# Kernel optimization log

Measured on AMD Instinct MI355X. Metric: run time of the kernel, lower is better.

Reference implementation:

```python
import jax, jax.numpy as jnp
import numpy as np

FS = 50000000.0
PI = jnp.pi


def _scale_matrix(alpha, kW, n_pad):
    """kW x kW matrix equal to torch linear-interp (align_corners=False)
    kW -> N -> kW with N = round(kW / clamp(alpha, 0.001)), N bounded by n_pad."""
    a = jnp.maximum(alpha, 0.001)
    N = jnp.clip(jnp.round(kW / a), 1, n_pad).astype(jnp.int32)
    Nf = N.astype(jnp.float32)
    eye_k = jnp.eye(kW, dtype=jnp.float32)
    eye_n = jnp.eye(n_pad, dtype=jnp.float32)
    # down-sample matrix D: length kW -> N (rows j >= N masked to 0)
    j = jnp.arange(n_pad, dtype=jnp.float32)
    c = jnp.maximum((j + 0.5) * (kW / Nf) - 0.5, 0.0)
    i0f = jnp.floor(c)
    w1 = c - i0f
    i0 = jnp.clip(i0f.astype(jnp.int32), 0, kW - 1)
    i1 = jnp.minimum(i0 + 1, kW - 1)
    D = (1.0 - w1)[:, None] * eye_k[i0] + w1[:, None] * eye_k[i1]
    D = D * (jnp.arange(n_pad) < N)[:, None]
    # up-sample matrix U: length N -> kW (reads only cols < N)
    i = jnp.arange(kW, dtype=jnp.float32)
    c2 = jnp.maximum((i + 0.5) * (Nf / kW) - 0.5, 0.0)
    j0 = jnp.floor(c2).astype(jnp.int32)
    j1 = jnp.minimum(j0 + 1, N - 1)
    w2 = c2 - j0.astype(jnp.float32)
    U = (1.0 - w2)[:, None] * eye_n[j0] + w2[:, None] * eye_n[j1]
    return U @ D  # [kW, kW]


def _mix_phase(w, phi):
    # w: [B,OC,2,1,kW], phi: [B,kW]; complex rotation of (I,Q) channel pair
    I, Q = w[:, :, 0, 0, :], w[:, :, 1, 0, :]
    c, sn = jnp.cos(phi)[:, None, :], jnp.sin(phi)[:, None, :]
    return jnp.stack([I * c - Q * sn, I * sn + Q * c], axis=2)[:, :, :, None, :]


def _steered_kernels(z, s, base_w, B):
    OC, IC, _, kW = base_w.shape
    n_pad = 2 * kW
    sf = jnp.nan_to_num(s)
    act = z > 0
    pick = lambda idx, neutral: jnp.where(act[:, idx], sf[:, idx], neutral)
    wB = jnp.broadcast_to(base_w[None], (B, OC, IC, 1, kW))
    # SCALE (PERTURB_ORDER idx 1)
    alpha = pick(1, 1.0)
    M = jax.vmap(lambda a: _scale_matrix(a, kW, n_pad))(alpha)  # [B,kW,kW]
    wB = jnp.einsum('bij,bocuj->bocui', M, wB)
    # CFO (idx 0) then CHIRP (idx 4): sequential phase rotations = summed phase
    n = jnp.arange(kW, dtype=jnp.float32)
    phi = 2.0 * PI * pick(0, 0.0)[:, None] * n[None, :] / FS
    t = n / FS
    phi = phi + PI * pick(4, 0.0)[:, None] * (t ** 2)[None, :]
    wB = _mix_phase(wB, phi)
    # GAIN (idx 2)
    wB = pick(2, 1.0)[:, None, None, None, None] * wB
    # SHIFT (idx 3): per-sample circular roll, out[i] = in[(i - s) mod kW]
    sh = jnp.round(pick(3, 0.0)).astype(jnp.int32)
    idx = (jnp.arange(kW)[None, :] - sh[:, None]) % kW  # [B,kW]
    idx = jnp.broadcast_to(idx[:, None, None, None, :], wB.shape)
    wB = jnp.take_along_axis(wB, idx, axis=-1)
    return wB  # [B,OC,2,1,kW]


def reference(x, z, s, base_w):
    B, IC, _, L = x.shape
    OC, _, _, kW = base_w.shape
    wB = _steered_kernels(z, s, base_w, B)
    xG = x.reshape(1, B * IC, 1, L)
    wG = wB.reshape(B * OC, IC, 1, kW)
    y = jax.lax.conv_general_dilated(
        xG, wG, window_strides=(1, 1), padding=[(0, 0), (kW // 2, kW // 2)],
        dimension_numbers=('NCHW', 'OIHW', 'NCHW'), feature_group_count=B)
    return y.reshape(B, OC, 1, L)


def setup_inputs() -> dict:
    key = jax.random.key(0)
    ks = jax.random.split(key, 4)
    B, OC, IC, kW, L = 32, 64, 2, 65, 65536
    x = jax.random.normal(ks[0], (B, IC, 1, L), dtype=jnp.float32)
    base_w = jax.random.normal(ks[1], (OC, IC, 1, kW), dtype=jnp.float32) * 0.1
    z = jax.random.randint(ks[2], (B, 5), 0, 2).astype(jnp.int32)
    u = jax.random.uniform(ks[3], (B, 5), dtype=jnp.float32)
    f0 = (u[:, 0] * 2.0 - 1.0) * 1.0e5         # CFO in +/-100 kHz
    alpha = 0.75 + u[:, 1] * 0.65               # SCALE in [0.75, 1.4]
    gain = 0.5 + u[:, 2]                        # GAIN in [0.5, 1.5]
    shift = jnp.round((u[:, 3] * 2.0 - 1.0) * 3.0)  # SHIFT integer in [-3, 3]
    chirp = (u[:, 4] * 2.0 - 1.0) * 1.0e12      # CHIRP rate
    s = jnp.stack([f0, alpha, gain, shift, chirp], axis=1)
    return {"x": x, "z": z, "s": s, "base_w": base_w}
```

## Files before the change

kernel.cpp:

```cpp
#include <hip/hip_runtime.h>
#include <math.h>

#define KW 65
#define L_LEN 65536
#define B_N 32
#define OC_N 64
#define KPAD 160
#define SEC 80
#define LT 256
#define XBASE 344

typedef __attribute__((ext_vector_type(8))) short short8;
typedef __attribute__((ext_vector_type(4))) float f32x4;

__device__ __forceinline__ unsigned short f2bf(float f) {
    unsigned u = __builtin_bit_cast(unsigned, f);
    unsigned r = u + 0x7FFFu + ((u >> 16) & 1u);
    return (unsigned short)(r >> 16);
}

__device__ __forceinline__ float nan0(float v) {
    if (isnan(v)) return 0.0f;
    if (isinf(v)) return v > 0.0f ? 3.4028234663852886e38f : -3.4028234663852886e38f;
    return v;
}

__global__ __launch_bounds__(256) void steer_weights(
        const int* __restrict__ z, const float* __restrict__ s,
        const float* __restrict__ bw, unsigned short* __restrict__ wpk) {
    const float PI = 3.14159265358979323846f;
    const float FS = 50000000.0f;
    int b = blockIdx.x;
    int t = threadIdx.x;

    const int*   zb = z + b * 5;
    const float* sb = s + b * 5;
    float f0    = (zb[0] > 0) ? nan0(sb[0]) : 0.0f;
    float alpha = (zb[1] > 0) ? nan0(sb[1]) : 1.0f;
    float gain  = (zb[2] > 0) ? nan0(sb[2]) : 1.0f;
    float shf   = (zb[3] > 0) ? nan0(sb[3]) : 0.0f;
    float chirp = (zb[4] > 0) ? nan0(sb[4]) : 0.0f;

    float a = fmaxf(alpha, 0.001f);
    float Nf_raw = rintf(65.0f / a);
    int   N  = (int)fminf(fmaxf(Nf_raw, 1.0f), 130.0f);
    float Nf = (float)N;
    int   sh = (int)rintf(shf);

    __shared__ float rw[OC_N][2][KW];
    __shared__ float cph[KW], sph[KW];

    if (t < KW) {
        float n  = (float)t;
        float tt = n / FS;
        float phi = 2.0f * PI * f0 * n / FS + PI * chirp * tt * tt;
        cph[t] = cosf(phi);
        sph[t] = sinf(phi);
    }
    if (t >= 128) {
        int oc = (t - 128) >> 1, ch = t & 1;
        const float* w = bw + (oc * 2 + ch) * KW;
        float KdivN = 65.0f / Nf;
        float NdivK = Nf / 65.0f;
        for (int i = 0; i < KW; ++i) {
            float c2  = fmaxf(((float)i + 0.5f) * NdivK - 0.5f, 0.0f);
            float j0f = floorf(c2);
            int   j0  = (int)j0f;
            int   j1  = min(j0 + 1, N - 1);
            float w2  = c2 - j0f;
            float v0, v1;
            {
                float c   = fmaxf(((float)j0 + 0.5f) * KdivN - 0.5f, 0.0f);
                float i0f = floorf(c);
                int   i0  = min((int)i0f, KW - 1);
                int   i1  = min(i0 + 1, KW - 1);
                float w1  = c - i0f;
                v0 = (1.0f - w1) * w[i0] + w1 * w[i1];
            }
            {
                float c   = fmaxf(((float)j1 + 0.5f) * KdivN - 0.5f, 0.0f);
                float i0f = floorf(c);
                int   i0  = min((int)i0f, KW - 1);
                int   i1  = min(i0 + 1, KW - 1);
                float w1  = c - i0f;
                v1 = (1.0f - w1) * w[i0] + w1 * w[i1];
            }
            rw[oc][ch][i] = (1.0f - w2) * v0 + w2 * v1;
        }
    }
    __syncthreads();
    {
        int oc = t >> 2, q = t & 3;
        unsigned short* ob = wpk + ((size_t)b * OC_N + oc) * KPAD;
        int sh0 = ((sh % KW) + KW) % KW;
        int k0 = 17 * q, k1 = min(KW, k0 + 17);
        for (int k = k0; k < k1; ++k) {
            float I = rw[oc][0][k], Q = rw[oc][1][k];
            float cp = cph[k], sp = sph[k];
            float Ip = (I * cp - Q * sp) * gain;
            float Qp = (I * sp + Q * cp) * gain;
            int kk = k + sh0; if (kk >= KW) kk -= KW;
            ob[kk]       = f2bf(Ip);
            ob[SEC + kk] = f2bf(Qp);
        }
        if (q == 3) {
            for (int kk = KW; kk < SEC; ++kk) { ob[kk] = 0; ob[SEC + kk] = 0; }
        }
    }
}

__global__ __launch_bounds__(256, 3) void steer_conv_mfma(
        const float* __restrict__ x, const unsigned short* __restrict__ wpk,
        float* __restrict__ y) {
    int b   = blockIdx.y;
    int l0  = blockIdx.x * LT;
    int tid = threadIdx.x;
    int wv = tid >> 6, lane = tid & 63;
    int c = lane & 15, g = lane >> 4;
    int a = wv & 1, lsub = wv >> 1;

    __shared__ __align__(16) unsigned short xt[8][2][XBASE];

    short8 afr[2][5];
    #pragma unroll
    for (int ot = 0; ot < 2; ++ot) {
        const unsigned short* wb = wpk + ((size_t)b * OC_N + 32 * a + 16 * ot + c) * KPAD;
        #pragma unroll
        for (int s = 0; s < 5; ++s)
            afr[ot][s] = *(const short8*)(wb + 32 * s + 8 * g);
    }

    const float* xb = x + (size_t)b * 2 * L_LEN;

    if (tid < 172) {
        int ch = tid / 86, i4 = tid % 86;
        int gi = l0 - 32 + 4 * i4;
        float4 v;
        if (gi >= 0 && gi + 3 < L_LEN) {
            v = *(const float4*)(xb + (size_t)ch * L_LEN + gi);
        } else {
            float tmp[4];
            #pragma unroll
            for (int u = 0; u < 4; ++u) {
                int q = gi + u;
                tmp[u] = (q >= 0 && q < L_LEN) ? xb[(size_t)ch * L_LEN + q] : 0.0f;
            }
            v = make_float4(tmp[0], tmp[1], tmp[2], tmp[3]);
        }
        unsigned r0 = (unsigned)f2bf(v.x) | ((unsigned)f2bf(v.y) << 16);
        unsigned r1 = (unsigned)f2bf(v.z) | ((unsigned)f2bf(v.w) << 16);
        *(uint2*)&xt[0][ch][4 * i4] = make_uint2(r0, r1);
    }
    __syncthreads();

    if (tid < 84) {
        int ch = tid / 42, j = tid % 42;
        const unsigned* src = (const unsigned*)&xt[0][ch][8 * j];
        unsigned d[8];
        #pragma unroll
        for (int i = 0; i < 8; ++i) d[i] = src[i];
        #pragma unroll
        for (int p = 1; p < 8; ++p) {
            int q = p >> 1;
            unsigned o[4];
            #pragma unroll
            for (int i = 0; i < 4; ++i)
                o[i] = (p & 1) ? ((d[i + q] >> 16) | (d[i + q + 1] << 16)) : d[i + q];
            *(uint4*)&xt[p][ch][8 * j] = make_uint4(o[0], o[1], o[2], o[3]);
        }
    }

    int boff[5];
    #pragma unroll
    for (int s = 0; s < 5; ++s) {
        int k0 = 32 * s + 8 * g;
        int ch = (k0 >= SEC) ? 1 : 0;
        int t0 = k0 - SEC * ch;
        boff[s] = ch * XBASE + 128 * lsub + 8 * c + t0;
    }
    __syncthreads();

    f32x4 acc[2][8];
    #pragma unroll
    for (int ot = 0; ot < 2; ++ot)
        #pragma unroll
        for (int p = 0; p < 8; ++p) acc[ot][p] = (f32x4){0.f, 0.f, 0.f, 0.f};

    #pragma unroll
    for (int p = 0; p < 8; ++p) {
        const unsigned short* xp = &xt[p][0][0];
        #pragma unroll
        for (int s = 0; s < 5; ++s) {
            short8 bfr = *(const short8*)(xp + boff[s]);
            acc[0][p] = __builtin_amdgcn_mfma_f32_16x16x32_bf16(afr[0][s], bfr, acc[0][p], 0, 0, 0);
            acc[1][p] = __builtin_amdgcn_mfma_f32_16x16x32_bf16(afr[1][s], bfr, acc[1][p], 0, 0, 0);
        }
    }

    #pragma unroll
    for (int ot = 0; ot < 2; ++ot) {
        #pragma unroll
        for (int r = 0; r < 4; ++r) {
            int oc = 32 * a + 16 * ot + 4 * g + r;
            float* yr = y + ((size_t)b * OC_N + oc) * L_LEN + l0 + 128 * lsub + 8 * c;
            f32x4 lo = { acc[ot][0][r], acc[ot][1][r], acc[ot][2][r], acc[ot][3][r] };
            f32x4 hi = { acc[ot][4][r], acc[ot][5][r], acc[ot][6][r], acc[ot][7][r] };
            *(f32x4*)yr       = lo;
            *((f32x4*)yr + 1) = hi;
        }
    }
}

extern "C" void kernel_launch(void* const* d_in, const int* in_sizes, int n_in,
                              void* d_out, int out_size, void* d_ws, size_t ws_size,
                              hipStream_t stream) {
    const float* x  = (const float*)d_in[0];
    const int*   z  = (const int*)d_in[1];
    const float* s  = (const float*)d_in[2];
    const float* bw = (const float*)d_in[3];
    float* y = (float*)d_out;
    unsigned short* wpk = (unsigned short*)d_ws;

    steer_weights<<<dim3(B_N), dim3(256), 0, stream>>>(z, s, bw, wpk);
    steer_conv_mfma<<<dim3(L_LEN / LT, B_N), dim3(256), 0, stream>>>(x, wpk, y);
}
```

Before: 147.3 us.

## Loop conv blocks over four tiles with prefetch and parallelize weight resampling

Each conv block now processes four consecutive 256-sample tiles in a loop. The input LDS buffer is double-buffered, and the global load for the next tile is issued by the non-shift threads while the shift/pack step of the current tile runs, so per-block setup (weight fragment loads) is amortized and input fetch latency overlaps other work. The weight kernel precomputes interpolation index and weight tables in shared memory, then spreads the 128x65 resampling over all 256 threads instead of a 65-step serial loop on 128 threads. The cost is a quarter as many conv blocks and more LDS per block.

After: 142.2 us. 3.5% less time.

```diff
diff --git a/kernel.cpp b/kernel.cpp
--- a/kernel.cpp
+++ b/kernel.cpp
@@ -8,6 +8,8 @@
 #define KPAD 160
 #define SEC 80
 #define LT 256
+#define NT 4
+#define LGRP (LT*NT)
 #define XBASE 344
 
 typedef __attribute__((ext_vector_type(8))) short short8;
@@ -49,6 +51,10 @@
 
     __shared__ float rw[OC_N][2][KW];
     __shared__ float cph[KW], sph[KW];
+    __shared__ int   j0t[KW], j1t[KW];
+    __shared__ float w2t[KW];
+    __shared__ int   i0t[130], i1t[130];
+    __shared__ float w1t[130];
 
     if (t < KW) {
         float n  = (float)t;
@@ -56,39 +62,32 @@
         float phi = 2.0f * PI * f0 * n / FS + PI * chirp * tt * tt;
         cph[t] = cosf(phi);
         sph[t] = sinf(phi);
-    }
-    if (t >= 128) {
-        int oc = (t - 128) >> 1, ch = t & 1;
-        const float* w = bw + (oc * 2 + ch) * KW;
-        float KdivN = 65.0f / Nf;
-        float NdivK = Nf / 65.0f;
-        for (int i = 0; i < KW; ++i) {
-            float c2  = fmaxf(((float)i + 0.5f) * NdivK - 0.5f, 0.0f);
-            float j0f = floorf(c2);
-            int   j0  = (int)j0f;
-            int   j1  = min(j0 + 1, N - 1);
-            float w2  = c2 - j0f;
-            float v0, v1;
-            {
-                float c   = fmaxf(((float)j0 + 0.5f) * KdivN - 0.5f, 0.0f);
-                float i0f = floorf(c);
-                int   i0  = min((int)i0f, KW - 1);
-                int   i1  = min(i0 + 1, KW - 1);
-                float w1  = c - i0f;
-                v0 = (1.0f - w1) * w[i0] + w1 * w[i1];
-            }
-            {
-                float c   = fmaxf(((float)j1 + 0.5f) * KdivN - 0.5f, 0.0f);
-                float i0f = floorf(c);
-                int   i0  = min((int)i0f, KW - 1);
-                int   i1  = min(i0 + 1, KW - 1);
-                float w1  = c - i0f;
-                v1 = (1.0f - w1) * w[i0] + w1 * w[i1];
-            }
-            rw[oc][ch][i] = (1.0f - w2) * v0 + w2 * v1;
-        }
+        float c2  = fmaxf(((float)t + 0.5f) * (Nf / 65.0f) - 0.5f, 0.0f);
+        float j0f = floorf(c2);
+        j0t[t] = (int)j0f;
+        j1t[t] = min((int)j0f + 1, N - 1);
+        w2t[t] = c2 - j0f;
+    } else if (t < KW + 130) {
+        int j = t - KW;
+        float c   = fmaxf(((float)j + 0.5f) * (65.0f / Nf) - 0.5f, 0.0f);
+        float i0f = floorf(c);
+        int   i0  = min((int)i0f, KW - 1);
+        i0t[j] = i0;
+        i1t[j] = min(i0 + 1, KW - 1);
+        w1t[j] = c - i0f;
     }
     __syncthreads();
+
+    for (int item = t; item < 128 * KW; item += 256) {
+        int row = item / KW, i = item % KW;
+        const float* w = bw + row * KW;
+        int j0 = j0t[i], j1 = j1t[i];
+        float v0 = (1.0f - w1t[j0]) * w[i0t[j0]] + w1t[j0] * w[i1t[j0]];
+        float v1 = (1.0f - w1t[j1]) * w[i0t[j1]] + w1t[j1] * w[i1t[j1]];
+        rw[row >> 1][row & 1][i] = (1.0f - w2t[i]) * v0 + w2t[i] * v1;
+    }
+    __syncthreads();
+
     {
         int oc = t >> 2, q = t & 3;
         unsigned short* ob = wpk + ((size_t)b * OC_N + oc) * KPAD;
@@ -113,13 +112,13 @@
         const float* __restrict__ x, const unsigned short* __restrict__ wpk,
         float* __restrict__ y) {
     int b   = blockIdx.y;
-    int l0  = blockIdx.x * LT;
+    int L0  = blockIdx.x * LGRP;
     int tid = threadIdx.x;
     int wv = tid >> 6, lane = tid & 63;
     int c = lane & 15, g = lane >> 4;
     int a = wv & 1, lsub = wv >> 1;
 
-    __shared__ __align__(16) unsigned short xt[8][2][XBASE];
+    __shared__ __align__(16) unsigned short xt[2][8][2][XBASE];
 
     short8 afr[2][5];
     #pragma unroll
@@ -132,43 +131,9 @@
 
     const float* xb = x + (size_t)b * 2 * L_LEN;
 
-    if (tid < 172) {
-        int ch = tid / 86, i4 = tid % 86;
-        int gi = l0 - 32 + 4 * i4;
-        float4 v;
-        if (gi >= 0 && gi + 3 < L_LEN) {
-            v = *(const float4*)(xb + (size_t)ch * L_LEN + gi);
-        } else {
-            float tmp[4];
-            #pragma unroll
-            for (int u = 0; u < 4; ++u) {
-                int q = gi + u;
-                tmp[u] = (q >= 0 && q < L_LEN) ? xb[(size_t)ch * L_LEN + q] : 0.0f;
-            }
-            v = make_float4(tmp[0], tmp[1], tmp[2], tmp[3]);
-        }
-        unsigned r0 = (unsigned)f2bf(v.x) | ((unsigned)f2bf(v.y) << 16);
-        unsigned r1 = (unsigned)f2bf(v.z) | ((unsigned)f2bf(v.w) << 16);
-        *(uint2*)&xt[0][ch][4 * i4] = make_uint2(r0, r1);
-    }
-    __syncthreads();
-
-    if (tid < 84) {
-        int ch = tid / 42, j = tid % 42;
-        const unsigned* src = (const unsigned*)&xt[0][ch][8 * j];
-        unsigned d[8];
-        #pragma unroll
-        for (int i = 0; i < 8; ++i) d[i] = src[i];
-        #pragma unroll
-        for (int p = 1; p < 8; ++p) {
-            int q = p >> 1;
-            unsigned o[4];
-            #pragma unroll
-            for (int i = 0; i < 4; ++i)
-                o[i] = (p & 1) ? ((d[i + q] >> 16) | (d[i + q + 1] << 16)) : d[i + q];
-            *(uint4*)&xt[p][ch][8 * j] = make_uint4(o[0], o[1], o[2], o[3]);
-        }
-    }
+    bool isLoader = (tid >= 84);
+    int lidx = tid - 84;
+    int lch = lidx / 86, li4 = lidx % 86;
 
     int boff[5];
     #pragma unroll
@@ -178,36 +143,93 @@
         int t0 = k0 - SEC * ch;
         boff[s] = ch * XBASE + 128 * lsub + 8 * c + t0;
     }
-    __syncthreads();
-
-    f32x4 acc[2][8];
-    #pragma unroll
-    for (int ot = 0; ot < 2; ++ot)
-        #pragma unroll
-        for (int p = 0; p < 8; ++p) acc[ot][p] = (f32x4){0.f, 0.f, 0.f, 0.f};
-
-    #pragma unroll
-    for (int p = 0; p < 8; ++p) {
-        const unsigned short* xp = &xt[p][0][0];
-        #pragma unroll
-        for (int s = 0; s < 5; ++s) {
-            short8 bfr = *(const short8*)(xp + boff[s]);
-            acc[0][p] = __builtin_amdgcn_mfma_f32_16x16x32_bf16(afr[0][s], bfr, acc[0][p], 0, 0, 0);
-            acc[1][p] = __builtin_amdgcn_mfma_f32_16x16x32_bf16(afr[1][s], bfr, acc[1][p], 0, 0, 0);
-        }
-    }
-
-    #pragma unroll
-    for (int ot = 0; ot < 2; ++ot) {
-        #pragma unroll
-        for (int r = 0; r < 4; ++r) {
-            int oc = 32 * a + 16 * ot + 4 * g + r;
-            float* yr = y + ((size_t)b * OC_N + oc) * L_LEN + l0 + 128 * lsub + 8 * c;
-            f32x4 lo = { acc[ot][0][r], acc[ot][1][r], acc[ot][2][r], acc[ot][3][r] };
-            f32x4 hi = { acc[ot][4][r], acc[ot][5][r], acc[ot][6][r], acc[ot][7][r] };
-            *(f32x4*)yr       = lo;
-            *((f32x4*)yr + 1) = hi;
-        }
+
+    float4 v;
+    if (isLoader) {
+        int gi = L0 - 32 + 4 * li4;
+        if (gi >= 0 && gi + 3 < L_LEN) {
+            v = *(const float4*)(xb + (size_t)lch * L_LEN + gi);
+        } else {
+            float tmp[4];
+            #pragma unroll
+            for (int u = 0; u < 4; ++u) {
+                int q = gi + u;
+                tmp[u] = (q >= 0 && q < L_LEN) ? xb[(size_t)lch * L_LEN + q] : 0.0f;
+            }
+            v = make_float4(tmp[0], tmp[1], tmp[2], tmp[3]);
+        }
+    }
+
+    int cur = 0;
+    for (int t = 0; t < NT; ++t) {
+        int l0 = L0 + t * LT;
+        if (isLoader) {
+            unsigned r0 = (unsigned)f2bf(v.x) | ((unsigned)f2bf(v.y) << 16);
+            unsigned r1 = (unsigned)f2bf(v.z) | ((unsigned)f2bf(v.w) << 16);
+            *(uint2*)&xt[cur][0][lch][4 * li4] = make_uint2(r0, r1);
+        }
+        __syncthreads();
+        if (tid < 84) {
+            int ch = tid / 42, j = tid % 42;
+            const unsigned* src = (const unsigned*)&xt[cur][0][ch][8 * j];
+            unsigned d[8];
+            #pragma unroll
+            for (int i = 0; i < 8; ++i) d[i] = src[i];
+            #pragma unroll
+            for (int p = 1; p < 8; ++p) {
+                int q = p >> 1;
+                unsigned o[4];
+                #pragma unroll
+                for (int i = 0; i < 4; ++i)
+                    o[i] = (p & 1) ? ((d[i + q] >> 16) | (d[i + q + 1] << 16)) : d[i + q];
+                *(uint4*)&xt[cur][p][ch][8 * j] = make_uint4(o[0], o[1], o[2], o[3]);
+            }
+        } else if (t + 1 < NT) {
+            int gi = L0 + (t + 1) * LT - 32 + 4 * li4;
+            if (gi >= 0 && gi + 3 < L_LEN) {
+                v = *(const float4*)(xb + (size_t)lch * L_LEN + gi);
+            } else {
+                float tmp[4];
+                #pragma unroll
+                for (int u = 0; u < 4; ++u) {
+                    int q = gi + u;
+                    tmp[u] = (q >= 0 && q < L_LEN) ? xb[(size_t)lch * L_LEN + q] : 0.0f;
+                }
+                v = make_float4(tmp[0], tmp[1], tmp[2], tmp[3]);
+            }
+        }
+        __syncthreads();
+
+        f32x4 acc[2][8];
+        #pragma unroll
+        for (int ot = 0; ot < 2; ++ot)
+            #pragma unroll
+            for (int p = 0; p < 8; ++p) acc[ot][p] = (f32x4){0.f, 0.f, 0.f, 0.f};
+
+        #pragma unroll
+        for (int p = 0; p < 8; ++p) {
+            const unsigned short* xp = &xt[cur][p][0][0];
+            #pragma unroll
+            for (int s = 0; s < 5; ++s) {
+                short8 bfr = *(const short8*)(xp + boff[s]);
+                acc[0][p] = __builtin_amdgcn_mfma_f32_16x16x32_bf16(afr[0][s], bfr, acc[0][p], 0, 0, 0);
+                acc[1][p] = __builtin_amdgcn_mfma_f32_16x16x32_bf16(afr[1][s], bfr, acc[1][p], 0, 0, 0);
+            }
+        }
+
+        #pragma unroll
+        for (int ot = 0; ot < 2; ++ot) {
+            #pragma unroll
+            for (int r = 0; r < 4; ++r) {
+                int oc = 32 * a + 16 * ot + 4 * g + r;
+                float* yr = y + ((size_t)b * OC_N + oc) * L_LEN + l0 + 128 * lsub + 8 * c;
+                f32x4 lo = { acc[ot][0][r], acc[ot][1][r], acc[ot][2][r], acc[ot][3][r] };
+                f32x4 hi = { acc[ot][4][r], acc[ot][5][r], acc[ot][6][r], acc[ot][7][r] };
+                *(f32x4*)yr       = lo;
+                *((f32x4*)yr + 1) = hi;
+            }
+        }
+        cur ^= 1;
     }
 }
 
@@ -222,5 +244,5 @@
     unsigned short* wpk = (unsigned short*)d_ws;
 
     steer_weights<<<dim3(B_N), dim3(256), 0, stream>>>(z, s, bw, wpk);
-    steer_conv_mfma<<<dim3(L_LEN / LT, B_N), dim3(256), 0, stream>>>(x, wpk, y);
-}
+    steer_conv_mfma<<<dim3(L_LEN / LGRP, B_N), dim3(256), 0, stream>>>(x, wpk, y);
+}
```
